# Kernel optimization log

Measured on AMD Instinct MI355X. Metric: run time of the kernel, lower is better.

The kernel has to match this reference:

```python
import jax, jax.numpy as jnp
import numpy as np

B, D, P = 8192, 256, 4096
TEMP = 0.5
MOMENTUM = 0.9
EPS = 1e-12  # matches torch F.normalize eps


def _l2_normalize(x):
    n = jnp.sqrt(jnp.sum(x * x, axis=1, keepdims=True))
    return x / jnp.maximum(n, EPS)


def setup_inputs() -> dict:
    key = jax.random.key(0)
    k1, k2, k3 = jax.random.split(key, 3)
    embeddings = jax.random.normal(k1, (B, D), dtype=jnp.float32)
    prototypes = jax.random.normal(k2, (P, D), dtype=jnp.float32)
    cluster_ids = jax.random.randint(k3, (B,), 0, P, dtype=jnp.int64)
    return {"embeddings": embeddings, "prototypes": prototypes, "cluster_ids": cluster_ids}


def reference(embeddings, prototypes, cluster_ids):
    cluster_ids = cluster_ids.astype(jnp.int32)
    emb_norm = _l2_normalize(embeddings)            # [B, D]
    proto_norm = _l2_normalize(prototypes)          # [P, D]
    sim = (emb_norm @ proto_norm.T) / TEMP          # [B, P]

    rows = jnp.arange(sim.shape[0])
    pos_sim = sim[rows, cluster_ids]                # [B]
    neg_sim = sim.at[rows, cluster_ids].set(-jnp.inf)
    # stable logsumexp over negatives (positive column masked out)
    max_val = jnp.max(neg_sim, axis=1, keepdims=True)
    lse = jnp.log(jnp.sum(jnp.exp(neg_sim - max_val), axis=1)) + max_val[:, 0]
    loss = jnp.mean(-pos_sim + lse)

    # serial per-sample EMA prototype update (faithful to the torch for-loop,
    # including sequential dependence on repeated cluster ids)
    def step(protos, xe):
        cid, e = xe
        new_row = MOMENTUM * protos[cid] + (1.0 - MOMENTUM) * e
        return protos.at[cid].set(new_row), None

    new_prototypes, _ = jax.lax.scan(step, prototypes, (cluster_ids, embeddings))
    return loss, new_prototypes
```

## Files before the change

kernel.cpp:

```cpp
#include <hip/hip_runtime.h>
#include <hip/hip_bf16.h>
#include <math.h>

#define Bn 8192
#define Dn 256
#define Pn 4096

using f16x8 = _Float16 __attribute__((ext_vector_type(8)));
using f16x4 = _Float16 __attribute__((ext_vector_type(4)));
using f32x16 = float __attribute__((ext_vector_type(16)));

__global__ void norm_rows_kernel(const float* __restrict__ emb, const float* __restrict__ protos,
                                 _Float16* __restrict__ embn, _Float16* __restrict__ pron,
                                 float* __restrict__ s_glob) {
    int gid  = blockIdx.x;
    int row  = gid * 4 + (threadIdx.x >> 6);
    int lane = threadIdx.x & 63;
    const float* in;
    _Float16* out;
    int r;
    if (row < Bn) { in = emb;    out = embn; r = row; }
    else          { in = protos; out = pron; r = row - Bn; }
    const float4 v = reinterpret_cast<const float4*>(in + (size_t)r * Dn)[lane];
    float ss = v.x * v.x + v.y * v.y + v.z * v.z + v.w * v.w;
#pragma unroll
    for (int m = 1; m <= 32; m <<= 1) ss += __shfl_xor(ss, m);
    float scale = 1.0f / fmaxf(sqrtf(ss), 1e-12f);
    f16x4 o;
    o[0] = (_Float16)(v.x * scale);
    o[1] = (_Float16)(v.y * scale);
    o[2] = (_Float16)(v.z * scale);
    o[3] = (_Float16)(v.w * scale);
    reinterpret_cast<f16x4*>(out + (size_t)r * Dn)[lane] = o;
    if (gid < Bn / 1024) s_glob[gid * 256 + threadIdx.x] = 0.0f;
}

__global__ __launch_bounds__(256, 2)
void gemm_expsum_kernel(const _Float16* __restrict__ embn, const _Float16* __restrict__ pron,
                        float* __restrict__ s_glob) {
    __shared__ _Float16 Bs[2][32 * Dn];
    const int w    = threadIdx.x >> 6;
    const int lane = threadIdx.x & 63;
    const int lo   = lane & 31;
    const int hi   = lane >> 5;
    const int rbase = blockIdx.x * 128 + w * 32;
    const int cbase = blockIdx.y * 256;

    const _Float16* ap = embn + (size_t)(rbase + lo) * Dn + hi * 8;
    f16x8 a[16];
#pragma unroll
    for (int kk = 0; kk < 16; ++kk)
        a[kk] = *reinterpret_cast<const f16x8*>(ap + kk * 16);

    float s[16];
#pragma unroll
    for (int r = 0; r < 16; ++r) s[r] = 0.0f;

    constexpr float K1 = 2.0f * 1.4426950408889634f;

    auto stage = [&](int sub, _Float16* buf) {
#pragma unroll
        for (int i = 0; i < 4; ++i) {
            int g = i * 4 + w;
            const _Float16* gsrc =
                pron + (size_t)(cbase + sub * 32 + lo) * Dn + g * 16 + hi * 8;
            char* l = (char*)buf + (g << 10);
            __builtin_amdgcn_global_load_lds(
                (const __attribute__((address_space(1))) unsigned int*)gsrc,
                (__attribute__((address_space(3))) unsigned int*)l, 16, 0, 0);
        }
    };

    stage(0, Bs[0]);
    __syncthreads();

    for (int sub = 0; sub < 8; ++sub) {
        const _Float16* cur = Bs[sub & 1];
        if (sub < 7) stage(sub + 1, Bs[(sub + 1) & 1]);

        f32x16 acc;
#pragma unroll
        for (int r = 0; r < 16; ++r) acc[r] = 0.0f;
#pragma unroll
        for (int kk = 0; kk < 16; ++kk) {
            f16x8 b = *reinterpret_cast<const f16x8*>(
                (const char*)cur + (kk << 10) + (lane << 4));
            acc = __builtin_amdgcn_mfma_f32_32x32x16_f16(a[kk], b, acc, 0, 0, 0);
        }
#pragma unroll
        for (int r = 0; r < 16; ++r)
            s[r] += exp2f(acc[r] * K1 - K1);

        __syncthreads();
    }

#pragma unroll
    for (int r = 0; r < 16; ++r) {
        float v = s[r];
        v += __shfl_xor(v, 1);
        v += __shfl_xor(v, 2);
        v += __shfl_xor(v, 4);
        v += __shfl_xor(v, 8);
        v += __shfl_xor(v, 16);
        if (lo == 0) {
            int row = rbase + (r & 3) + 8 * (r >> 2) + 4 * hi;
            atomicAdd(&s_glob[row], v);
        }
    }
}

__global__ void loss_kernel(const _Float16* __restrict__ embn, const _Float16* __restrict__ pron,
                            const int* __restrict__ cid, const float* __restrict__ s_glob,
                            float* __restrict__ terms) {
    int row  = blockIdx.x * 4 + (threadIdx.x >> 6);
    int lane = threadIdx.x & 63;
    int c = cid[row];
    f16x4 e = reinterpret_cast<const f16x4*>(embn + (size_t)row * Dn)[lane];
    f16x4 p = reinterpret_cast<const f16x4*>(pron + (size_t)c * Dn)[lane];
    float d = 0.0f;
#pragma unroll
    for (int j = 0; j < 4; ++j) d += (float)e[j] * (float)p[j];
#pragma unroll
    for (int m = 1; m <= 32; m <<= 1) d += __shfl_xor(d, m);
    if (lane == 0) {
        float pos  = d * 2.0f;
        float sneg = s_glob[row] - __expf(pos - 2.0f);
        float lse  = __logf(sneg) + 2.0f;
        terms[row] = lse - pos;
    }
}

__global__ void reduce_loss_kernel(const float* __restrict__ terms, float* __restrict__ loss) {
    int t = threadIdx.x;
    const float4* T = reinterpret_cast<const float4*>(terms);
    float s = 0.0f;
#pragma unroll
    for (int i = 0; i < Bn / 4 / 256; ++i) {
        float4 v = T[i * 256 + t];
        s += v.x + v.y + v.z + v.w;
    }
#pragma unroll
    for (int m = 1; m <= 32; m <<= 1) s += __shfl_xor(s, m);
    __shared__ float wsum[4];
    if ((t & 63) == 0) wsum[t >> 6] = s;
    __syncthreads();
    if (t == 0) loss[0] = (wsum[0] + wsum[1] + wsum[2] + wsum[3]) * (1.0f / (float)Bn);
}

__global__ void hist_kernel(const int* __restrict__ cid, int* __restrict__ hist) {
    __shared__ int h[Pn];
    for (int c = threadIdx.x; c < Pn; c += 256) h[c] = 0;
    __syncthreads();
    int i = blockIdx.x * 256 + threadIdx.x;
    atomicAdd(&h[cid[i]], 1);
    __syncthreads();
    for (int c = threadIdx.x; c < Pn; c += 256)
        hist[blockIdx.x * Pn + c] = h[c];
}

__global__ void counts_kernel(const int* __restrict__ hist, int* __restrict__ counts,
                              int* __restrict__ pref) {
    int c = blockIdx.x * 256 + threadIdx.x;
    int s = 0;
#pragma unroll
    for (int ch = 0; ch < 32; ++ch) {
        pref[ch * Pn + c] = s;
        s += hist[ch * Pn + c];
    }
    counts[c] = s;
}

__global__ void rank_kernel(const int* __restrict__ cid, const int* __restrict__ pref,
                            int* __restrict__ rank) {
    __shared__ int ids[256];
    int t = threadIdx.x;
    int i = blockIdx.x * 256 + t;
    ids[t] = cid[i];
    __syncthreads();
    int my = ids[t];
    int r = pref[blockIdx.x * Pn + my];
    for (int j = 0; j < t; ++j) r += (ids[j] == my) ? 1 : 0;
    rank[i] = r;
}

__global__ void offsets_kernel(const int* __restrict__ counts, int* __restrict__ offs) {
    __shared__ int wtot[4];
    int t = threadIdx.x;
    int local[16];
    int run = 0;
#pragma unroll
    for (int j = 0; j < 16; ++j) { local[j] = run; run += counts[t * 16 + j]; }
    int v = run;
#pragma unroll
    for (int d = 1; d < 64; d <<= 1) {
        int u = __shfl_up(v, d);
        if ((t & 63) >= d) v += u;
    }
    if ((t & 63) == 63) wtot[t >> 6] = v;
    __syncthreads();
    int add = 0;
    for (int ww = 0; ww < (t >> 6); ++ww) add += wtot[ww];
    int excl = add + v - run;
#pragma unroll
    for (int j = 0; j < 16; ++j) offs[t * 16 + j] = excl + local[j];
}

__global__ void fill_kernel(const int* __restrict__ cid, const int* __restrict__ rank,
                            const int* __restrict__ offs, int* __restrict__ slist) {
    int i = blockIdx.x * 256 + threadIdx.x;
    slist[offs[cid[i]] + rank[i]] = i;
}

__global__ void update_protos_kernel(const float* __restrict__ protos, const float* __restrict__ emb,
                                     const int* __restrict__ counts, const int* __restrict__ offs,
                                     const int* __restrict__ slist, float* __restrict__ outp) {
    int w = threadIdx.x >> 6, lane = threadIdx.x & 63;
    int c = blockIdx.x * 4 + w;
    int cnt = counts[c], off = offs[c];
    float4 p = reinterpret_cast<const float4*>(protos + (size_t)c * Dn)[lane];
    float scale = __powf(0.9f, (float)cnt);
    float4 acc;
    acc.x = p.x * scale; acc.y = p.y * scale; acc.z = p.z * scale; acc.w = p.w * scale;
    for (int j = 0; j < cnt; ++j) {
        int i = slist[off + j];
        float wgt = 0.1f * __powf(0.9f, (float)(cnt - 1 - j));
        float4 e = reinterpret_cast<const float4*>(emb + (size_t)i * Dn)[lane];
        acc.x += wgt * e.x; acc.y += wgt * e.y; acc.z += wgt * e.z; acc.w += wgt * e.w;
    }
    reinterpret_cast<float4*>(outp + (size_t)c * Dn)[lane] = acc;
}

extern "C" void kernel_launch(void* const* d_in, const int* in_sizes, int n_in,
                              void* d_out, int out_size, void* d_ws, size_t ws_size,
                              hipStream_t stream) {
    const float* emb    = (const float*)d_in[0];
    const float* protos = (const float*)d_in[1];
    const int*   cid    = (const int*)d_in[2];
    float* out = (float*)d_out;

    char* ws = (char*)d_ws;
    _Float16* embn = (_Float16*)ws;
    _Float16* pron = (_Float16*)(ws + ((size_t)4 << 20));
    float* s_glob  = (float*)(ws + ((size_t)6 << 20));
    int*   counts  = (int*)(ws + ((size_t)6 << 20) + 32768);
    int*   rank    = (int*)(ws + ((size_t)6 << 20) + 49152);
    float* terms   = (float*)(ws + ((size_t)6 << 20) + 81920);
    int*   offs    = (int*)(ws + ((size_t)6 << 20) + 114688);
    int*   slist   = (int*)(ws + ((size_t)6 << 20) + 131072);
    int*   hist    = (int*)(ws + ((size_t)7 << 20));
    int*   pref    = (int*)(ws + ((size_t)7 << 20) + 524288);

    norm_rows_kernel<<<(Bn + Pn) / 4, 256, 0, stream>>>(emb, protos, embn, pron, s_glob);

    gemm_expsum_kernel<<<dim3(Bn / 128, Pn / 256), 256, 0, stream>>>(embn, pron, s_glob);
    loss_kernel<<<Bn / 4, 256, 0, stream>>>(embn, pron, cid, s_glob, terms);
    reduce_loss_kernel<<<1, 256, 0, stream>>>(terms, out);

    hist_kernel<<<Bn / 256, 256, 0, stream>>>(cid, hist);
    counts_kernel<<<Pn / 256, 256, 0, stream>>>(hist, counts, pref);
    rank_kernel<<<Bn / 256, 256, 0, stream>>>(cid, pref, rank);
    offsets_kernel<<<1, 256, 0, stream>>>(counts, offs);
    fill_kernel<<<Bn / 256, 256, 0, stream>>>(cid, rank, offs, slist);
    update_protos_kernel<<<Pn / 4, 256, 0, stream>>>(protos, emb, counts, offs, slist, out + 1);
}
```

Measured before the change: 129.0 us.

## Fuse small kernels and mask positive column inside GEMM epilogue

Cuts the launch count from ten to five. The histogram moves into the normalization kernel, and counts, prefix and offsets are merged into one scan kernel. Rank computation and list fill are merged too. The GEMM epilogue now skips the positive column and writes its similarity, which removes the separate loss kernel, and the final loss reduction runs in block 0 of the prototype update kernel. This trades per-kernel launch and serialization overhead for extra compare and branch work in the GEMM epilogue and a serial 8192-element reduction in a single block.

```diff
diff --git a/kernel.cpp b/kernel.cpp
--- a/kernel.cpp
+++ b/kernel.cpp
@@ -10,10 +10,16 @@
 using f16x4 = _Float16 __attribute__((ext_vector_type(4)));
 using f32x16 = float __attribute__((ext_vector_type(16)));
 
-__global__ void norm_rows_kernel(const float* __restrict__ emb, const float* __restrict__ protos,
+__global__ void norm_hist_kernel(const float* __restrict__ emb, const float* __restrict__ protos,
+                                 const int* __restrict__ cid,
                                  _Float16* __restrict__ embn, _Float16* __restrict__ pron,
-                                 float* __restrict__ s_glob) {
+                                 float* __restrict__ s_glob, int* __restrict__ hist) {
+    __shared__ int h[Pn];
     int gid  = blockIdx.x;
+    bool do_hist = (gid < Bn / 256);
+    if (do_hist)
+        for (int c = threadIdx.x; c < Pn; c += 256) h[c] = 0;
+
     int row  = gid * 4 + (threadIdx.x >> 6);
     int lane = threadIdx.x & 63;
     const float* in;
@@ -32,12 +38,64 @@
     o[2] = (_Float16)(v.z * scale);
     o[3] = (_Float16)(v.w * scale);
     reinterpret_cast<f16x4*>(out + (size_t)r * Dn)[lane] = o;
+
     if (gid < Bn / 1024) s_glob[gid * 256 + threadIdx.x] = 0.0f;
+
+    if (do_hist) {
+        __syncthreads();
+        atomicAdd(&h[cid[gid * 256 + threadIdx.x]], 1);
+        __syncthreads();
+        for (int c = threadIdx.x; c < Pn; c += 256)
+            hist[gid * Pn + c] = h[c];
+    }
+}
+
+__global__ __launch_bounds__(1024)
+void prefscan_kernel(const int* __restrict__ hist, int* __restrict__ pref,
+                     int* __restrict__ offs) {
+    __shared__ int wt[16];
+    int t = threadIdx.x;
+    int4 run = {0, 0, 0, 0};
+    for (int ch = 0; ch < 32; ++ch) {
+        int4 v = reinterpret_cast<const int4*>(hist + ch * Pn)[t];
+        reinterpret_cast<int4*>(pref + ch * Pn)[t] = run;
+        run.x += v.x; run.y += v.y; run.z += v.z; run.w += v.w;
+    }
+    int l1 = run.x, l2 = l1 + run.y, l3 = l2 + run.z;
+    int tot = l3 + run.w;
+    int v = tot;
+#pragma unroll
+    for (int d = 1; d < 64; d <<= 1) {
+        int u = __shfl_up(v, d);
+        if ((t & 63) >= d) v += u;
+    }
+    if ((t & 63) == 63) wt[t >> 6] = v;
+    __syncthreads();
+    int add = 0;
+    for (int ww = 0; ww < (t >> 6); ++ww) add += wt[ww];
+    int base = add + v - tot;
+    int4 o = {base, base + l1, base + l2, base + l3};
+    reinterpret_cast<int4*>(offs)[t] = o;
+    if (t == 0) offs[Pn] = Bn;
+}
+
+__global__ void rankfill_kernel(const int* __restrict__ cid, const int* __restrict__ pref,
+                                const int* __restrict__ offs, int* __restrict__ slist) {
+    __shared__ int ids[256];
+    int t = threadIdx.x, g = blockIdx.x;
+    int i = g * 256 + t;
+    int my = cid[i];
+    ids[t] = my;
+    __syncthreads();
+    int r = pref[g * Pn + my];
+    for (int j = 0; j < t; ++j) r += (ids[j] == my) ? 1 : 0;
+    slist[offs[my] + r] = i;
 }
 
 __global__ __launch_bounds__(256, 2)
 void gemm_expsum_kernel(const _Float16* __restrict__ embn, const _Float16* __restrict__ pron,
-                        float* __restrict__ s_glob) {
+                        const int* __restrict__ cid,
+                        float* __restrict__ s_glob, float* __restrict__ pos_glob) {
     __shared__ _Float16 Bs[2][32 * Dn];
     const int w    = threadIdx.x >> 6;
     const int lane = threadIdx.x & 63;
@@ -51,6 +109,11 @@
 #pragma unroll
     for (int kk = 0; kk < 16; ++kk)
         a[kk] = *reinterpret_cast<const f16x8*>(ap + kk * 16);
+
+    int cidr[16];
+#pragma unroll
+    for (int r = 0; r < 16; ++r)
+        cidr[r] = cid[rbase + (r & 3) + 8 * (r >> 2) + 4 * hi];
 
     float s[16];
 #pragma unroll
@@ -87,10 +150,15 @@
                 (const char*)cur + (kk << 10) + (lane << 4));
             acc = __builtin_amdgcn_mfma_f32_32x32x16_f16(a[kk], b, acc, 0, 0, 0);
         }
-#pragma unroll
-        for (int r = 0; r < 16; ++r)
-            s[r] += exp2f(acc[r] * K1 - K1);
-
+        int colv = cbase + sub * 32 + lo;
+#pragma unroll
+        for (int r = 0; r < 16; ++r) {
+            float e = exp2f(fmaf(acc[r], K1, -K1));
+            bool ispos = (cidr[r] == colv);
+            s[r] += ispos ? 0.0f : e;
+            if (ispos)
+                pos_glob[rbase + (r & 3) + 8 * (r >> 2) + 4 * hi] = acc[r] * 2.0f;
+        }
         __syncthreads();
     }
 
@@ -109,114 +177,15 @@
     }
 }
 
-__global__ void loss_kernel(const _Float16* __restrict__ embn, const _Float16* __restrict__ pron,
-                            const int* __restrict__ cid, const float* __restrict__ s_glob,
-                            float* __restrict__ terms) {
-    int row  = blockIdx.x * 4 + (threadIdx.x >> 6);
-    int lane = threadIdx.x & 63;
-    int c = cid[row];
-    f16x4 e = reinterpret_cast<const f16x4*>(embn + (size_t)row * Dn)[lane];
-    f16x4 p = reinterpret_cast<const f16x4*>(pron + (size_t)c * Dn)[lane];
-    float d = 0.0f;
-#pragma unroll
-    for (int j = 0; j < 4; ++j) d += (float)e[j] * (float)p[j];
-#pragma unroll
-    for (int m = 1; m <= 32; m <<= 1) d += __shfl_xor(d, m);
-    if (lane == 0) {
-        float pos  = d * 2.0f;
-        float sneg = s_glob[row] - __expf(pos - 2.0f);
-        float lse  = __logf(sneg) + 2.0f;
-        terms[row] = lse - pos;
-    }
-}
-
-__global__ void reduce_loss_kernel(const float* __restrict__ terms, float* __restrict__ loss) {
-    int t = threadIdx.x;
-    const float4* T = reinterpret_cast<const float4*>(terms);
-    float s = 0.0f;
-#pragma unroll
-    for (int i = 0; i < Bn / 4 / 256; ++i) {
-        float4 v = T[i * 256 + t];
-        s += v.x + v.y + v.z + v.w;
-    }
-#pragma unroll
-    for (int m = 1; m <= 32; m <<= 1) s += __shfl_xor(s, m);
-    __shared__ float wsum[4];
-    if ((t & 63) == 0) wsum[t >> 6] = s;
-    __syncthreads();
-    if (t == 0) loss[0] = (wsum[0] + wsum[1] + wsum[2] + wsum[3]) * (1.0f / (float)Bn);
-}
-
-__global__ void hist_kernel(const int* __restrict__ cid, int* __restrict__ hist) {
-    __shared__ int h[Pn];
-    for (int c = threadIdx.x; c < Pn; c += 256) h[c] = 0;
-    __syncthreads();
-    int i = blockIdx.x * 256 + threadIdx.x;
-    atomicAdd(&h[cid[i]], 1);
-    __syncthreads();
-    for (int c = threadIdx.x; c < Pn; c += 256)
-        hist[blockIdx.x * Pn + c] = h[c];
-}
-
-__global__ void counts_kernel(const int* __restrict__ hist, int* __restrict__ counts,
-                              int* __restrict__ pref) {
-    int c = blockIdx.x * 256 + threadIdx.x;
-    int s = 0;
-#pragma unroll
-    for (int ch = 0; ch < 32; ++ch) {
-        pref[ch * Pn + c] = s;
-        s += hist[ch * Pn + c];
-    }
-    counts[c] = s;
-}
-
-__global__ void rank_kernel(const int* __restrict__ cid, const int* __restrict__ pref,
-                            int* __restrict__ rank) {
-    __shared__ int ids[256];
-    int t = threadIdx.x;
-    int i = blockIdx.x * 256 + t;
-    ids[t] = cid[i];
-    __syncthreads();
-    int my = ids[t];
-    int r = pref[blockIdx.x * Pn + my];
-    for (int j = 0; j < t; ++j) r += (ids[j] == my) ? 1 : 0;
-    rank[i] = r;
-}
-
-__global__ void offsets_kernel(const int* __restrict__ counts, int* __restrict__ offs) {
-    __shared__ int wtot[4];
-    int t = threadIdx.x;
-    int local[16];
-    int run = 0;
-#pragma unroll
-    for (int j = 0; j < 16; ++j) { local[j] = run; run += counts[t * 16 + j]; }
-    int v = run;
-#pragma unroll
-    for (int d = 1; d < 64; d <<= 1) {
-        int u = __shfl_up(v, d);
-        if ((t & 63) >= d) v += u;
-    }
-    if ((t & 63) == 63) wtot[t >> 6] = v;
-    __syncthreads();
-    int add = 0;
-    for (int ww = 0; ww < (t >> 6); ++ww) add += wtot[ww];
-    int excl = add + v - run;
-#pragma unroll
-    for (int j = 0; j < 16; ++j) offs[t * 16 + j] = excl + local[j];
-}
-
-__global__ void fill_kernel(const int* __restrict__ cid, const int* __restrict__ rank,
-                            const int* __restrict__ offs, int* __restrict__ slist) {
-    int i = blockIdx.x * 256 + threadIdx.x;
-    slist[offs[cid[i]] + rank[i]] = i;
-}
-
-__global__ void update_protos_kernel(const float* __restrict__ protos, const float* __restrict__ emb,
-                                     const int* __restrict__ counts, const int* __restrict__ offs,
-                                     const int* __restrict__ slist, float* __restrict__ outp) {
+__global__ void update_loss_kernel(const float* __restrict__ protos, const float* __restrict__ emb,
+                                   const int* __restrict__ offs, const int* __restrict__ slist,
+                                   const float* __restrict__ s_glob, const float* __restrict__ pos_glob,
+                                   float* __restrict__ out) {
+    __shared__ float ws2[4];
+    float* outp = out + 1;
     int w = threadIdx.x >> 6, lane = threadIdx.x & 63;
     int c = blockIdx.x * 4 + w;
-    int cnt = counts[c], off = offs[c];
+    int off = offs[c], cnt = offs[c + 1] - off;
     float4 p = reinterpret_cast<const float4*>(protos + (size_t)c * Dn)[lane];
     float scale = __powf(0.9f, (float)cnt);
     float4 acc;
@@ -228,6 +197,18 @@
         acc.x += wgt * e.x; acc.y += wgt * e.y; acc.z += wgt * e.z; acc.w += wgt * e.w;
     }
     reinterpret_cast<float4*>(outp + (size_t)c * Dn)[lane] = acc;
+
+    if (blockIdx.x == 0) {
+        float ssum = 0.0f;
+        for (int i = threadIdx.x; i < Bn; i += 256)
+            ssum += __logf(s_glob[i]) + 2.0f - pos_glob[i];
+#pragma unroll
+        for (int m = 1; m <= 32; m <<= 1) ssum += __shfl_xor(ssum, m);
+        if ((threadIdx.x & 63) == 0) ws2[threadIdx.x >> 6] = ssum;
+        __syncthreads();
+        if (threadIdx.x == 0)
+            out[0] = (ws2[0] + ws2[1] + ws2[2] + ws2[3]) * (1.0f / (float)Bn);
+    }
 }
 
 extern "C" void kernel_launch(void* const* d_in, const int* in_sizes, int n_in,
@@ -242,24 +223,15 @@
     _Float16* embn = (_Float16*)ws;
     _Float16* pron = (_Float16*)(ws + ((size_t)4 << 20));
     float* s_glob  = (float*)(ws + ((size_t)6 << 20));
-    int*   counts  = (int*)(ws + ((size_t)6 << 20) + 32768);
-    int*   rank    = (int*)(ws + ((size_t)6 << 20) + 49152);
-    float* terms   = (float*)(ws + ((size_t)6 << 20) + 81920);
-    int*   offs    = (int*)(ws + ((size_t)6 << 20) + 114688);
-    int*   slist   = (int*)(ws + ((size_t)6 << 20) + 131072);
+    float* pos_g   = (float*)(ws + ((size_t)6 << 20) + 32768);
+    int*   offs    = (int*)(ws + ((size_t)6 << 20) + 65536);
+    int*   slist   = (int*)(ws + ((size_t)6 << 20) + 98304);
     int*   hist    = (int*)(ws + ((size_t)7 << 20));
     int*   pref    = (int*)(ws + ((size_t)7 << 20) + 524288);
 
-    norm_rows_kernel<<<(Bn + Pn) / 4, 256, 0, stream>>>(emb, protos, embn, pron, s_glob);
-
-    gemm_expsum_kernel<<<dim3(Bn / 128, Pn / 256), 256, 0, stream>>>(embn, pron, s_glob);
-    loss_kernel<<<Bn / 4, 256, 0, stream>>>(embn, pron, cid, s_glob, terms);
-    reduce_loss_kernel<<<1, 256, 0, stream>>>(terms, out);
-
-    hist_kernel<<<Bn / 256, 256, 0, stream>>>(cid, hist);
-    counts_kernel<<<Pn / 256, 256, 0, stream>>>(hist, counts, pref);
-    rank_kernel<<<Bn / 256, 256, 0, stream>>>(cid, pref, rank);
-    offsets_kernel<<<1, 256, 0, stream>>>(counts, offs);
-    fill_kernel<<<Bn / 256, 256, 0, stream>>>(cid, rank, offs, slist);
-    update_protos_kernel<<<Pn / 4, 256, 0, stream>>>(protos, emb, counts, offs, slist, out + 1);
-}
+    norm_hist_kernel<<<(Bn + Pn) / 4, 256, 0, stream>>>(emb, protos, cid, embn, pron, s_glob, hist);
+    prefscan_kernel<<<1, 1024, 0, stream>>>(hist, pref, offs);
+    rankfill_kernel<<<Bn / 256, 256, 0, stream>>>(cid, pref, offs, slist);
+    gemm_expsum_kernel<<<dim3(Bn / 128, Pn / 256), 256, 0, stream>>>(embn, pron, cid, s_glob, pos_g);
+    update_loss_kernel<<<Pn / 4, 256, 0, stream>>>(protos, emb, offs, slist, s_glob, pos_g, out);
+}
```

Result: slower. 142.3 us (+10.3%).
